# Kernel optimization log

Hardware: AMD Instinct MI355X
Metric: run time of the kernel (lower is better)

## Reference

```python
import jax, jax.numpy as jnp
import numpy as np

T, B, DIM, N = 2048, 16, 1024, 64


def setup_inputs() -> dict:
    key = jax.random.key(0)
    ks = jax.random.split(key, 6)
    # xavier-uniform-ish scale for [N, DIM] linear weights
    lim = float(np.sqrt(6.0 / (DIM + N)))
    mk = lambda k: jax.random.uniform(k, (N, DIM), jnp.float32, -lim, lim)
    return {
        "x": jax.random.normal(ks[0], (T, B, DIM), jnp.float32),
        "S": jnp.zeros((B, N, N), jnp.float32),
        "W_k": mk(ks[1]),
        "W_v": mk(ks[2]),
        "W_q": mk(ks[3]),
        "W_alpha": mk(ks[4]),
        "d_alpha": jnp.full((N,), 0.1, jnp.float32),
        "b_alpha": jnp.full((N,), 2.0, jnp.float32),
    }


def reference(x, S, W_k, W_v, W_q, W_alpha, d_alpha, b_alpha):
    # Projections for the whole sequence at once: [T, B, N]
    k_all = jnp.einsum('tbd,nd->tbn', x, W_k)
    v_all = jnp.einsum('tbd,nd->tbn', x, W_v)
    q_all = jnp.einsum('tbd,nd->tbn', x, W_q)
    a_all = jnp.einsum('tbd,nd->tbn', x, W_alpha)

    def step(S, inp):
        k, v, q, ax = inp  # each [B, N]
        retrieved = jnp.einsum('bij,bj->bi', S, k)                 # [B, N]
        alpha = jax.nn.sigmoid(ax + d_alpha * retrieved + b_alpha)  # [B, N]
        outer_vk = v[:, :, None] * k[:, None, :]                    # [B, N, N]
        S = alpha[:, :, None] * S + (1.0 - alpha[:, :, None]) * outer_vk
        out = jnp.einsum('bij,bj->bi', S, q)                        # [B, N]
        out = out * jax.nn.silu(out)
        return S, out

    S_final, output = jax.lax.scan(step, S, (k_all, v_all, q_all, a_all))
    return output, S_final
```

## Files before the change

kernel.cpp:

```cpp
#include <hip/hip_runtime.h>
#include <hip/hip_bf16.h>

#define T_STEPS 2048
#define BATCH 16
#define DIM 1024
#define NDIM 64
#define M_TOTAL (T_STEPS * BATCH)
#define STRIDE (BATCH * NDIM)
#define CH 32

typedef __attribute__((ext_vector_type(8))) short bf16x8;
typedef __attribute__((ext_vector_type(4))) float f32x4;
typedef __attribute__((ext_vector_type(2))) float f32x2;

#define NEG_LOG2E -1.44269504088896f

__device__ inline unsigned pk_bf(float lo, float hi) {
    __hip_bfloat162 h = __float22bfloat162_rn(float2{lo, hi});
    return *(unsigned*)&h;
}

template <int CTRL>
__device__ inline float dpp_add(float x) {
    int v = __builtin_amdgcn_update_dpp(0, __float_as_int(x), CTRL, 0xF, 0xF, true);
    return x + __int_as_float(v);
}
__device__ inline float red16(float x) {
    x = dpp_add<0xB1>(x);
    x = dpp_add<0x4E>(x);
    x = dpp_add<0x141>(x);
    x = dpp_add<0x140>(x);
    return x;
}
__device__ inline void red16x2(float& a, float& b) {
    a = dpp_add<0xB1>(a);  b = dpp_add<0xB1>(b);
    a = dpp_add<0x4E>(a);  b = dpp_add<0x4E>(b);
    a = dpp_add<0x141>(a); b = dpp_add<0x141>(b);
    a = dpp_add<0x140>(a); b = dpp_add<0x140>(b);
}
__device__ inline float dot4(f32x4 a, f32x4 b) {
    f32x2 t = a.lo * b.lo;
    t = a.hi * b.hi + t;
    return t.x + t.y;
}
__device__ inline float silu_o(float o) {
    float e = __builtin_amdgcn_exp2f(o * NEG_LOG2E);
    return o * o * __builtin_amdgcn_rcpf(1.f + e);
}

#define AS1 __attribute__((address_space(1)))
#define AS3 __attribute__((address_space(3)))
__device__ inline void gl_lds16(const float* g, float* l) {
    __builtin_amdgcn_global_load_lds((const AS1 unsigned*)g, (AS3 unsigned*)l, 16, 0, 0);
}
__device__ inline void gl_lds4(const float* g, float* l) {
    __builtin_amdgcn_global_load_lds((const AS1 unsigned*)g, (AS3 unsigned*)l, 4, 0, 0);
}
#define WAIT_VM0 do { __builtin_amdgcn_s_waitcnt(0x0F70); asm volatile("" ::: "memory"); } while (0)

__global__ __launch_bounds__(256, 2) void proj_kernel(
    const float* __restrict__ x,
    const float* __restrict__ Wk, const float* __restrict__ Wq,
    const float* __restrict__ Wv, const float* __restrict__ Wa,
    const float* __restrict__ ba, float* __restrict__ Kp, float* __restrict__ Qp,
    float* __restrict__ VAi, float* __restrict__ kq) {
    __shared__ float sA[128 * 64];
    __shared__ float sB[128 * 64];

    const int m0 = blockIdx.x * 128;
    const int ntile = blockIdx.y;
    const int tid = threadIdx.x;
    const int wv = tid >> 6, lane = tid & 63, lrow = lane & 15, quad = lane >> 4;
    const int wm = wv & 1, wn = wv >> 1;

    const float* w0 = (ntile == 0) ? Wk : Wv;
    const float* w1 = (ntile == 0) ? Wq : Wa;

    f32x4 acc[4][4];
#pragma unroll
    for (int a = 0; a < 4; a++)
#pragma unroll
        for (int b = 0; b < 4; b++) acc[a][b] = (f32x4)(0.f);

    const float* xg = x + (size_t)(m0 + (tid >> 4)) * DIM + (tid & 15) * 4;
    const int wrow = tid >> 4, wcol = (tid & 15) * 4;

    for (int it = 0; it < 16; ++it) {
        const int k0 = it * 64;
        __syncthreads();
#pragma unroll
        for (int j = 0; j < 8; ++j)
            gl_lds16(xg + (size_t)(16 * j) * DIM + k0, &sA[(tid + 256 * j) * 4]);
#pragma unroll
        for (int j = 0; j < 4; ++j)
            gl_lds16(w0 + (size_t)(16 * j + wrow) * DIM + k0 + wcol, &sB[(tid + 256 * j) * 4]);
#pragma unroll
        for (int j = 0; j < 4; ++j)
            gl_lds16(w1 + (size_t)(16 * j + wrow) * DIM + k0 + wcol, &sB[(tid + 256 * (j + 4)) * 4]);
        WAIT_VM0;
        __syncthreads();

#pragma unroll
        for (int ks = 0; ks < 2; ++ks) {
            bf16x8 af[4];
#pragma unroll
            for (int mt = 0; mt < 4; ++mt) {
                const float* pa = &sA[(wm * 64 + mt * 16 + lrow) * 64 + ks * 32 + quad * 8];
                float4 lo = ((const float4*)pa)[0], hi = ((const float4*)pa)[1];
                unsigned pk[4] = {pk_bf(lo.x, lo.y), pk_bf(lo.z, lo.w),
                                  pk_bf(hi.x, hi.y), pk_bf(hi.z, hi.w)};
                af[mt] = *(bf16x8*)pk;
            }
#pragma unroll
            for (int nt = 0; nt < 4; ++nt) {
                const float* pb = &sB[(wn * 64 + nt * 16 + lrow) * 64 + ks * 32 + quad * 8];
                float4 lo = ((const float4*)pb)[0], hi = ((const float4*)pb)[1];
                unsigned pk[4] = {pk_bf(lo.x, lo.y), pk_bf(lo.z, lo.w),
                                  pk_bf(hi.x, hi.y), pk_bf(hi.z, hi.w)};
                bf16x8 bfr = *(bf16x8*)pk;
#pragma unroll
                for (int mt = 0; mt < 4; ++mt)
                    acc[mt][nt] = __builtin_amdgcn_mfma_f32_16x16x32_bf16(af[mt], bfr, acc[mt][nt], 0, 0, 0);
            }
        }
    }

    const int g2 = ntile * 2 + wn;
    float bav[4];
    if (g2 == 3) {
#pragma unroll
        for (int nt = 0; nt < 4; ++nt) bav[nt] = ba[nt * 16 + lrow];
    }
#pragma unroll
    for (int mt = 0; mt < 4; ++mt)
#pragma unroll
        for (int nt = 0; nt < 4; ++nt) {
            int col = nt * 16 + lrow;
#pragma unroll
            for (int reg = 0; reg < 4; ++reg) {
                int m = m0 + wm * 64 + mt * 16 + quad * 4 + reg;
                float vvv = acc[mt][nt][reg];
                if (g2 == 0) Kp[(size_t)m * 64 + col] = vvv;
                else if (g2 == 1) Qp[(size_t)m * 64 + col] = vvv;
                else if (g2 == 2) VAi[(size_t)m * 128 + col * 2] = vvv;
                else VAi[(size_t)m * 128 + col * 2 + 1] = NEG_LOG2E * (vvv + bav[nt]);
            }
        }

    if (ntile == 0) {
        __syncthreads();
        float* dst = (wn == 0) ? sA : sB;
#pragma unroll
        for (int mt = 0; mt < 4; ++mt)
#pragma unroll
            for (int nt = 0; nt < 4; ++nt)
#pragma unroll
                for (int reg = 0; reg < 4; ++reg)
                    dst[(wm * 64 + mt * 16 + quad * 4 + reg) * 64 + nt * 16 + lrow] =
                        acc[mt][nt][reg];
        __syncthreads();
        if (tid < 128) {
            float s = 0.f;
#pragma unroll
            for (int k4 = 0; k4 < 16; ++k4)
                s += dot4(*(const f32x4*)&sA[tid * 64 + k4 * 4],
                          *(const f32x4*)&sB[tid * 64 + k4 * 4]);
            kq[m0 + tid] = s;
        }
    }
}

__global__ __launch_bounds__(64, 1) void recur_kernel(
    const float* __restrict__ Kp, const float* __restrict__ Qp,
    const float* __restrict__ VAi, const float* __restrict__ KQp,
    const float* __restrict__ S0, const float* __restrict__ d_alpha,
    float* __restrict__ out, float* __restrict__ Sout) {
    __shared__ float Kl[2][CH][64];
    __shared__ float Ql[2][CH][64];
    __shared__ float VAl[2][CH][8];
    __shared__ float KQl[2][64];
    __shared__ float OlT[4][CH];

    int b = blockIdx.y, g = blockIdx.x, lane = threadIdx.x;
    int r = lane >> 4, c = lane & 15, i = g * 4 + r, c4 = c * 4;

    f32x4 sv = *(const f32x4*)(S0 + ((size_t)b * NDIM + i) * NDIM + c4);
    float da2 = d_alpha[i] * NEG_LOG2E;

    const float* Kbase = Kp + (size_t)b * NDIM + (size_t)(lane >> 4) * STRIDE + (lane & 15) * 4;
    const float* Qbase = Qp + (size_t)b * NDIM + (size_t)(lane >> 4) * STRIDE + (lane & 15) * 4;
    const float* VAbase = VAi + (size_t)b * 128 + g * 8 + (lane & 1) * 4 + (size_t)(lane >> 1) * 2048;
    const float* KQbase = KQp + b + (size_t)(lane & 31) * BATCH;

    auto load_chunk = [&](int t0, int buf) {
#pragma unroll
        for (int j = 0; j < 8; ++j) {
            gl_lds16(Kbase + (size_t)(t0 + j * 4) * STRIDE, &Kl[buf][j * 4][0]);
            gl_lds16(Qbase + (size_t)(t0 + j * 4) * STRIDE, &Ql[buf][j * 4][0]);
        }
        gl_lds16(VAbase + (size_t)t0 * 2048, &VAl[buf][0][0]);
        gl_lds4(KQbase + (size_t)t0 * BATCH, &KQl[buf][0]);
    };

    f32x4 kg[2][4], qg[2][4], kqg[2];
    f32x2 vg[2][4];
    f32x4 og;

#define LOADG(gi, buf, t4_) do {                                         \
    const float* Kb_ = &Kl[buf][0][0] + (t4_) * 64 + c4;                 \
    const float* Qb_ = &Ql[buf][0][0] + (t4_) * 64 + c4;                 \
    _Pragma("unroll")                                                    \
    for (int u_ = 0; u_ < 4; ++u_) {                                     \
        kg[gi][u_] = *(const f32x4*)(Kb_ + u_ * 64);                     \
        qg[gi][u_] = *(const f32x4*)(Qb_ + u_ * 64);                     \
        vg[gi][u_] = *(const f32x2*)(&VAl[buf][0][0] + ((t4_) + u_) * 8 + r * 2); \
    }                                                                    \
    kqg[gi] = *(const f32x4*)(&KQl[buf][0] + (t4_));                     \
} while (0)

#define STEP(gi, u) do {                                                 \
    f32x4 kv_ = kg[gi][u], qv_ = qg[gi][u];                              \
    f32x2 vva_ = vg[gi][u];                                              \
    float kqs_ = kqg[gi][u];                                             \
    f32x2 pk_ = kv_.lo * sv.lo; pk_ = kv_.hi * sv.hi + pk_;              \
    f32x2 pq_ = qv_.lo * sv.lo; pq_ = qv_.hi * sv.hi + pq_;              \
    float rk_ = pk_.x + pk_.y, rq_ = pq_.x + pq_.y;                      \
    red16x2(rk_, rq_);                                                   \
    float v_ = vva_.x;                                                   \
    f32x4 w_ = v_ * kv_;                                                 \
    f32x4 d_ = sv - w_;                                                  \
    float alpha_ = __builtin_amdgcn_rcpf(                                \
        1.f + __builtin_amdgcn_exp2f(fmaf(da2, rk_, vva_.y)));           \
    sv = w_ + alpha_ * d_;                                               \
    float vkq_ = v_ * kqs_;                                              \
    og[u] = fmaf(alpha_, rq_ - vkq_, vkq_);                 \
} while (0)

    load_chunk(0, 0);
    WAIT_VM0;
    LOADG(0, 0, 0);

#pragma unroll 1
    for (int j = 0; j < T_STEPS / CH; ++j) {
        const int cb = j & 1, nb = cb ^ 1;
        if (j + 1 < T_STEPS / CH) load_chunk((j + 1) * CH, nb);

#pragma unroll 1
        for (int t8 = 0; t8 < CH; t8 += 8) {
            LOADG(1, cb, t8 + 4);
            STEP(0, 0); STEP(0, 1); STEP(0, 2); STEP(0, 3);
            if (c == 0) *(f32x4*)(&OlT[r][t8]) = og;
            if (t8 + 8 < CH) LOADG(0, cb, t8 + 8);
            STEP(1, 0); STEP(1, 1); STEP(1, 2); STEP(1, 3);
            if (c == 0) *(f32x4*)(&OlT[r][t8 + 4]) = og;
        }
        WAIT_VM0;

        if (lane < 32) {
            float4 t4o;
            t4o.x = silu_o(OlT[0][lane]);
            t4o.y = silu_o(OlT[1][lane]);
            t4o.z = silu_o(OlT[2][lane]);
            t4o.w = silu_o(OlT[3][lane]);
            *(float4*)(out + ((size_t)(j * CH + lane) * BATCH + b) * NDIM + g * 4) = t4o;
        }

        if (j + 1 < T_STEPS / CH) LOADG(0, nb, 0);
    }
#undef STEP
#undef LOADG

    *(float4*)(Sout + ((size_t)b * NDIM + i) * NDIM + c4) = float4{sv.x, sv.y, sv.z, sv.w};
}

extern "C" void kernel_launch(void* const* d_in, const int* in_sizes, int n_in,
                              void* d_out, int out_size, void* d_ws, size_t ws_size,
                              hipStream_t stream) {
    const float* x  = (const float*)d_in[0];
    const float* S0 = (const float*)d_in[1];
    const float* Wk = (const float*)d_in[2];
    const float* Wv = (const float*)d_in[3];
    const float* Wq = (const float*)d_in[4];
    const float* Wa = (const float*)d_in[5];
    const float* da = (const float*)d_in[6];
    const float* ba = (const float*)d_in[7];

    float* out = (float*)d_out;
    float* Sout = out + (size_t)T_STEPS * BATCH * NDIM;

    const size_t per = (size_t)M_TOTAL * NDIM;
    float* Kp  = (float*)d_ws;
    float* Qp  = Kp + per;
    float* VAi = Qp + per;
    float* kq  = VAi + 2 * per;

    proj_kernel<<<dim3(M_TOTAL / 128, 2), dim3(256), 0, stream>>>(
        x, Wk, Wq, Wv, Wa, ba, Kp, Qp, VAi, kq);
    recur_kernel<<<dim3(16, BATCH), dim3(64), 0, stream>>>(Kp, Qp, VAi, kq, S0, da, out, Sout);
}
```

Measured before the change: 451.2 us.

## Shorten recurrence critical path via k·k' lookahead and pre-packed bf16 weights

Reformulates the recurrence so that the next step's retrieval S_{t+1}k_{t+1} comes from the alpha of the current step plus precomputed dot products. It uses k_t·k_{t+1} and k·q scalars from a new kq_kernel. This lets the exp for the next alpha be issued before the state update, taking the reduction off the serial dependency chain. Weights are also converted to bf16 once in a separate pack kernel, so the projection GEMM loads half the B bytes and skips per-tile conversion. The cost is two extra kernel launches and extra workspace traffic.

```diff
diff --git a/kernel.cpp b/kernel.cpp
--- a/kernel.cpp
+++ b/kernel.cpp
@@ -8,6 +8,7 @@
 #define M_TOTAL (T_STEPS * BATCH)
 #define STRIDE (BATCH * NDIM)
 #define CH 32
+#define NC (T_STEPS / CH)
 
 typedef __attribute__((ext_vector_type(8))) short bf16x8;
 typedef __attribute__((ext_vector_type(4))) float f32x4;
@@ -38,11 +39,6 @@
     a = dpp_add<0x141>(a); b = dpp_add<0x141>(b);
     a = dpp_add<0x140>(a); b = dpp_add<0x140>(b);
 }
-__device__ inline float dot4(f32x4 a, f32x4 b) {
-    f32x2 t = a.lo * b.lo;
-    t = a.hi * b.hi + t;
-    return t.x + t.y;
-}
 __device__ inline float silu_o(float o) {
     float e = __builtin_amdgcn_exp2f(o * NEG_LOG2E);
     return o * o * __builtin_amdgcn_rcpf(1.f + e);
@@ -53,19 +49,35 @@
 __device__ inline void gl_lds16(const float* g, float* l) {
     __builtin_amdgcn_global_load_lds((const AS1 unsigned*)g, (AS3 unsigned*)l, 16, 0, 0);
 }
+__device__ inline void gl_lds16s(const unsigned short* g, unsigned short* l) {
+    __builtin_amdgcn_global_load_lds((const AS1 unsigned*)g, (AS3 unsigned*)l, 16, 0, 0);
+}
 __device__ inline void gl_lds4(const float* g, float* l) {
     __builtin_amdgcn_global_load_lds((const AS1 unsigned*)g, (AS3 unsigned*)l, 4, 0, 0);
 }
 #define WAIT_VM0 do { __builtin_amdgcn_s_waitcnt(0x0F70); asm volatile("" ::: "memory"); } while (0)
 
-__global__ __launch_bounds__(256, 2) void proj_kernel(
-    const float* __restrict__ x,
+__global__ __launch_bounds__(256) void pack_w(
     const float* __restrict__ Wk, const float* __restrict__ Wq,
     const float* __restrict__ Wv, const float* __restrict__ Wa,
+    unsigned short* __restrict__ Wb) {
+    int n = blockIdx.x;
+    int sel = n >> 6;
+    const float* W = (sel == 0) ? Wk : (sel == 1) ? Wq : (sel == 2) ? Wv : Wa;
+    int k4 = threadIdx.x * 4;
+    float4 f = *(const float4*)(W + (size_t)(n & 63) * DIM + k4);
+    uint2 u;
+    u.x = pk_bf(f.x, f.y);
+    u.y = pk_bf(f.z, f.w);
+    *(uint2*)(Wb + (size_t)n * DIM + k4) = u;
+}
+
+__global__ __launch_bounds__(256, 2) void proj_kernel(
+    const float* __restrict__ x, const unsigned short* __restrict__ Wb,
     const float* __restrict__ ba, float* __restrict__ Kp, float* __restrict__ Qp,
-    float* __restrict__ VAi, float* __restrict__ kq) {
+    float* __restrict__ VAi) {
     __shared__ float sA[128 * 64];
-    __shared__ float sB[128 * 64];
+    __shared__ unsigned short sB[128 * 64];
 
     const int m0 = blockIdx.x * 128;
     const int ntile = blockIdx.y;
@@ -73,9 +85,6 @@
     const int wv = tid >> 6, lane = tid & 63, lrow = lane & 15, quad = lane >> 4;
     const int wm = wv & 1, wn = wv >> 1;
 
-    const float* w0 = (ntile == 0) ? Wk : Wv;
-    const float* w1 = (ntile == 0) ? Wq : Wa;
-
     f32x4 acc[4][4];
 #pragma unroll
     for (int a = 0; a < 4; a++)
@@ -83,7 +92,7 @@
         for (int b = 0; b < 4; b++) acc[a][b] = (f32x4)(0.f);
 
     const float* xg = x + (size_t)(m0 + (tid >> 4)) * DIM + (tid & 15) * 4;
-    const int wrow = tid >> 4, wcol = (tid & 15) * 4;
+    const unsigned short* wg = Wb + (size_t)(ntile * 128 + (tid >> 3)) * DIM + (tid & 7) * 8;
 
     for (int it = 0; it < 16; ++it) {
         const int k0 = it * 64;
@@ -93,10 +102,7 @@
             gl_lds16(xg + (size_t)(16 * j) * DIM + k0, &sA[(tid + 256 * j) * 4]);
 #pragma unroll
         for (int j = 0; j < 4; ++j)
-            gl_lds16(w0 + (size_t)(16 * j + wrow) * DIM + k0 + wcol, &sB[(tid + 256 * j) * 4]);
-#pragma unroll
-        for (int j = 0; j < 4; ++j)
-            gl_lds16(w1 + (size_t)(16 * j + wrow) * DIM + k0 + wcol, &sB[(tid + 256 * (j + 4)) * 4]);
+            gl_lds16s(wg + (size_t)(32 * j) * DIM + k0, &sB[(tid + 256 * j) * 8]);
         WAIT_VM0;
         __syncthreads();
 
@@ -113,11 +119,7 @@
             }
 #pragma unroll
             for (int nt = 0; nt < 4; ++nt) {
-                const float* pb = &sB[(wn * 64 + nt * 16 + lrow) * 64 + ks * 32 + quad * 8];
-                float4 lo = ((const float4*)pb)[0], hi = ((const float4*)pb)[1];
-                unsigned pk[4] = {pk_bf(lo.x, lo.y), pk_bf(lo.z, lo.w),
-                                  pk_bf(hi.x, hi.y), pk_bf(hi.z, hi.w)};
-                bf16x8 bfr = *(bf16x8*)pk;
+                bf16x8 bfr = *(const bf16x8*)&sB[(wn * 64 + nt * 16 + lrow) * 64 + ks * 32 + quad * 8];
 #pragma unroll
                 for (int mt = 0; mt < 4; ++mt)
                     acc[mt][nt] = __builtin_amdgcn_mfma_f32_16x16x32_bf16(af[mt], bfr, acc[mt][nt], 0, 0, 0);
@@ -146,39 +148,34 @@
                 else VAi[(size_t)m * 128 + col * 2 + 1] = NEG_LOG2E * (vvv + bav[nt]);
             }
         }
-
-    if (ntile == 0) {
-        __syncthreads();
-        float* dst = (wn == 0) ? sA : sB;
-#pragma unroll
-        for (int mt = 0; mt < 4; ++mt)
-#pragma unroll
-            for (int nt = 0; nt < 4; ++nt)
-#pragma unroll
-                for (int reg = 0; reg < 4; ++reg)
-                    dst[(wm * 64 + mt * 16 + quad * 4 + reg) * 64 + nt * 16 + lrow] =
-                        acc[mt][nt][reg];
-        __syncthreads();
-        if (tid < 128) {
-            float s = 0.f;
-#pragma unroll
-            for (int k4 = 0; k4 < 16; ++k4)
-                s += dot4(*(const f32x4*)&sA[tid * 64 + k4 * 4],
-                          *(const f32x4*)&sB[tid * 64 + k4 * 4]);
-            kq[m0 + tid] = s;
-        }
-    }
+}
+
+__global__ __launch_bounds__(256) void kq_kernel(
+    const float* __restrict__ Kp, const float* __restrict__ Qp,
+    float* __restrict__ kq, float* __restrict__ kk) {
+    int m = blockIdx.x * 16 + (threadIdx.x >> 4);
+    int c = threadIdx.x & 15;
+    float4 k = *(const float4*)(Kp + (size_t)m * 64 + c * 4);
+    float4 q = *(const float4*)(Qp + (size_t)m * 64 + c * 4);
+    float4 kn = {0.f, 0.f, 0.f, 0.f};
+    if (m + BATCH < M_TOTAL) kn = *(const float4*)(Kp + (size_t)(m + BATCH) * 64 + c * 4);
+    float pq = k.x * q.x + k.y * q.y + k.z * q.z + k.w * q.w;
+    float pk = k.x * kn.x + k.y * kn.y + k.z * kn.z + k.w * kn.w;
+    red16x2(pq, pk);
+    if (c == 0) { kq[m] = pq; kk[m] = pk; }
 }
 
 __global__ __launch_bounds__(64, 1) void recur_kernel(
     const float* __restrict__ Kp, const float* __restrict__ Qp,
     const float* __restrict__ VAi, const float* __restrict__ KQp,
+    const float* __restrict__ KKp,
     const float* __restrict__ S0, const float* __restrict__ d_alpha,
     float* __restrict__ out, float* __restrict__ Sout) {
     __shared__ float Kl[2][CH][64];
     __shared__ float Ql[2][CH][64];
     __shared__ float VAl[2][CH][8];
     __shared__ float KQl[2][64];
+    __shared__ float KKl[2][64];
     __shared__ float OlT[4][CH];
 
     int b = blockIdx.y, g = blockIdx.x, lane = threadIdx.x;
@@ -191,6 +188,7 @@
     const float* Qbase = Qp + (size_t)b * NDIM + (size_t)(lane >> 4) * STRIDE + (lane & 15) * 4;
     const float* VAbase = VAi + (size_t)b * 128 + g * 8 + (lane & 1) * 4 + (size_t)(lane >> 1) * 2048;
     const float* KQbase = KQp + b + (size_t)(lane & 31) * BATCH;
+    const float* KKbase = KKp + b + (size_t)(lane & 31) * BATCH;
 
     auto load_chunk = [&](int t0, int buf) {
 #pragma unroll
@@ -200,61 +198,99 @@
         }
         gl_lds16(VAbase + (size_t)t0 * 2048, &VAl[buf][0][0]);
         gl_lds4(KQbase + (size_t)t0 * BATCH, &KQl[buf][0]);
+        gl_lds4(KKbase + (size_t)t0 * BATCH, &KKl[buf][0]);
     };
 
-    f32x4 kg[2][4], qg[2][4], kqg[2];
+    f32x4 kg[2][4], qg[2][4], kqg[2], kkg[2];
     f32x2 vg[2][4];
     f32x4 og;
-
-#define LOADG(gi, buf, t4_) do {                                         \
-    const float* Kb_ = &Kl[buf][0][0] + (t4_) * 64 + c4;                 \
-    const float* Qb_ = &Ql[buf][0][0] + (t4_) * 64 + c4;                 \
-    _Pragma("unroll")                                                    \
-    for (int u_ = 0; u_ < 4; ++u_) {                                     \
-        kg[gi][u_] = *(const f32x4*)(Kb_ + u_ * 64);                     \
-        qg[gi][u_] = *(const f32x4*)(Qb_ + u_ * 64);                     \
+    float ee, ckm, rqm, vkk, vkq, v_cur;
+
+#define LOADG(gi, buf, t4_) do {                                          \
+    const float* Kb_ = &Kl[buf][0][0] + (t4_) * 64 + c4;                  \
+    const float* Qb_ = &Ql[buf][0][0] + (t4_) * 64 + c4;                  \
+    _Pragma("unroll")                                                     \
+    for (int u_ = 0; u_ < 4; ++u_) {                                      \
+        kg[gi][u_] = *(const f32x4*)(Kb_ + u_ * 64);                      \
+        qg[gi][u_] = *(const f32x4*)(Qb_ + u_ * 64);                      \
         vg[gi][u_] = *(const f32x2*)(&VAl[buf][0][0] + ((t4_) + u_) * 8 + r * 2); \
-    }                                                                    \
-    kqg[gi] = *(const f32x4*)(&KQl[buf][0] + (t4_));                     \
+    }                                                                     \
+    kqg[gi] = *(const f32x4*)(&KQl[buf][0] + (t4_));                      \
+    kkg[gi] = *(const f32x4*)(&KKl[buf][0] + (t4_));                      \
 } while (0)
 
-#define STEP(gi, u) do {                                                 \
-    f32x4 kv_ = kg[gi][u], qv_ = qg[gi][u];                              \
-    f32x2 vva_ = vg[gi][u];                                              \
-    float kqs_ = kqg[gi][u];                                             \
-    f32x2 pk_ = kv_.lo * sv.lo; pk_ = kv_.hi * sv.hi + pk_;              \
-    f32x2 pq_ = qv_.lo * sv.lo; pq_ = qv_.hi * sv.hi + pq_;              \
-    float rk_ = pk_.x + pk_.y, rq_ = pq_.x + pq_.y;                      \
-    red16x2(rk_, rq_);                                                   \
-    float v_ = vva_.x;                                                   \
-    f32x4 w_ = v_ * kv_;                                                 \
-    f32x4 d_ = sv - w_;                                                  \
-    float alpha_ = __builtin_amdgcn_rcpf(                                \
-        1.f + __builtin_amdgcn_exp2f(fmaf(da2, rk_, vva_.y)));           \
-    sv = w_ + alpha_ * d_;                                               \
-    float vkq_ = v_ * kqs_;                                              \
-    og[u] = fmaf(alpha_, rq_ - vkq_, vkq_);                 \
+#define STEP(u, kt_, kt2_, qt1_, vt1_, kqt1_, kkt1_) do {                 \
+    float alpha_ = __builtin_amdgcn_rcpf(1.f + ee);                       \
+    float rk1_ = fmaf(alpha_, ckm, vkk);                 \
+    ee = __builtin_amdgcn_exp2f(fmaf(da2, rk1_, (vt1_).y));               \
+    float o_ = fmaf(alpha_, rqm, vkq);                       \
+    f32x4 w_ = v_cur * (kt_);                                             \
+    f32x4 d_ = sv - w_;                                                   \
+    sv = w_ + alpha_ * d_;                                       \
+    f32x2 pq_ = (qt1_).lo * sv.lo; pq_ = (qt1_).hi * sv.hi + pq_;         \
+    f32x2 pk_ = (kt2_).lo * sv.lo; pk_ = (kt2_).hi * sv.hi + pk_;         \
+    float rq_ = pq_.x + pq_.y, ck_ = pk_.x + pk_.y;                       \
+    red16x2(rq_, ck_);                                  \
+    float v1_ = (vt1_).x;                                                 \
+    vkq = v1_ * (kqt1_); vkk = v1_ * (kkt1_);                             \
+    rqm = rq_ - vkq; ckm = ck_ - vkk;                                     \
+    og[u] = o_;                                                           \
+    v_cur = v1_;                                                          \
+} while (0)
+
+#define GROUP_A() do {                                                          \
+    STEP(0, kg[0][0], kg[0][2], qg[0][1], vg[0][1], kqg[0][1], kkg[0][1]);      \
+    STEP(1, kg[0][1], kg[0][3], qg[0][2], vg[0][2], kqg[0][2], kkg[0][2]);      \
+    STEP(2, kg[0][2], kg[1][0], qg[0][3], vg[0][3], kqg[0][3], kkg[0][3]);      \
+    STEP(3, kg[0][3], kg[1][1], qg[1][0], vg[1][0], kqg[1][0], kkg[1][0]);      \
+} while (0)
+#define GROUP_B() do {                                                          \
+    STEP(0, kg[1][0], kg[1][2], qg[1][1], vg[1][1], kqg[1][1], kkg[1][1]);      \
+    STEP(1, kg[1][1], kg[1][3], qg[1][2], vg[1][2], kqg[1][2], kkg[1][2]);      \
+    STEP(2, kg[1][2], kg[0][0], qg[1][3], vg[1][3], kqg[1][3], kkg[1][3]);      \
+    STEP(3, kg[1][3], kg[0][1], qg[0][0], vg[0][0], kqg[0][0], kkg[0][0]);      \
 } while (0)
 
     load_chunk(0, 0);
     WAIT_VM0;
     LOADG(0, 0, 0);
+    {
+        f32x2 p0 = kg[0][0].lo * sv.lo; p0 = kg[0][0].hi * sv.hi + p0;
+        f32x2 p1 = qg[0][0].lo * sv.lo; p1 = qg[0][0].hi * sv.hi + p1;
+        f32x2 p2 = kg[0][1].lo * sv.lo; p2 = kg[0][1].hi * sv.hi + p2;
+        float rk0 = p0.x + p0.y, rq0 = p1.x + p1.y, ck0 = p2.x + p2.y;
+        red16x2(rk0, rq0);
+        ck0 = red16(ck0);
+        float v0 = vg[0][0].x;
+        ee = __builtin_amdgcn_exp2f(fmaf(da2, rk0, vg[0][0].y));
+        vkq = v0 * kqg[0][0];
+        vkk = v0 * kkg[0][0];
+        rqm = rq0 - vkq;
+        ckm = ck0 - vkk;
+        v_cur = v0;
+    }
 
 #pragma unroll 1
-    for (int j = 0; j < T_STEPS / CH; ++j) {
+    for (int j = 0; j < NC; ++j) {
         const int cb = j & 1, nb = cb ^ 1;
-        if (j + 1 < T_STEPS / CH) load_chunk((j + 1) * CH, nb);
+        if (j + 1 < NC) load_chunk((j + 1) * CH, nb);
 
 #pragma unroll 1
-        for (int t8 = 0; t8 < CH; t8 += 8) {
+        for (int t8 = 0; t8 < 24; t8 += 8) {
             LOADG(1, cb, t8 + 4);
-            STEP(0, 0); STEP(0, 1); STEP(0, 2); STEP(0, 3);
+            GROUP_A();
             if (c == 0) *(f32x4*)(&OlT[r][t8]) = og;
-            if (t8 + 8 < CH) LOADG(0, cb, t8 + 8);
-            STEP(1, 0); STEP(1, 1); STEP(1, 2); STEP(1, 3);
+            LOADG(0, cb, t8 + 8);
+            GROUP_B();
             if (c == 0) *(f32x4*)(&OlT[r][t8 + 4]) = og;
         }
+        LOADG(1, cb, 28);
+        GROUP_A();
+        if (c == 0) *(f32x4*)(&OlT[r][24]) = og;
         WAIT_VM0;
+        LOADG(0, nb, 0);
+        GROUP_B();
+        if (c == 0) *(f32x4*)(&OlT[r][28]) = og;
 
         if (lane < 32) {
             float4 t4o;
@@ -264,9 +300,9 @@
             t4o.w = silu_o(OlT[3][lane]);
             *(float4*)(out + ((size_t)(j * CH + lane) * BATCH + b) * NDIM + g * 4) = t4o;
         }
-
-        if (j + 1 < T_STEPS / CH) LOADG(0, nb, 0);
     }
+#undef GROUP_A
+#undef GROUP_B
 #undef STEP
 #undef LOADG
 
@@ -293,8 +329,11 @@
     float* Qp  = Kp + per;
     float* VAi = Qp + per;
     float* kq  = VAi + 2 * per;
-
-    proj_kernel<<<dim3(M_TOTAL / 128, 2), dim3(256), 0, stream>>>(
-        x, Wk, Wq, Wv, Wa, ba, Kp, Qp, VAi, kq);
-    recur_kernel<<<dim3(16, BATCH), dim3(64), 0, stream>>>(Kp, Qp, VAi, kq, S0, da, out, Sout);
-}
+    float* kk  = kq + M_TOTAL;
+    unsigned short* Wb = (unsigned short*)(kk + M_TOTAL);
+
+    pack_w<<<dim3(256), dim3(256), 0, stream>>>(Wk, Wq, Wv, Wa, Wb);
+    proj_kernel<<<dim3(M_TOTAL / 128, 2), dim3(256), 0, stream>>>(x, Wb, ba, Kp, Qp, VAi);
+    kq_kernel<<<dim3(M_TOTAL / 16), dim3(256), 0, stream>>>(Kp, Qp, kq, kk);
+    recur_kernel<<<dim3(16, BATCH), dim3(64), 0, stream>>>(Kp, Qp, VAi, kq, kk, S0, da, out, Sout);
+}
```

Result: no change. 446.1 us (-1.1%).
